# Optimization experiments

Measured on AMD Instinct MI355X. Metric: run time of the kernel, lower is better.

The kernel has to match this reference:

```python
import jax, jax.numpy as jnp
import numpy as np

P = 7    # pool size (hard-coded in module)
DS = 16  # downsample rate


def _hat_int(t):
    # antiderivative of the bilinear hat kernel max(0, 1-|t|)
    t = jnp.clip(t, -1.0, 1.0)
    return jnp.where(t < 0, 0.5 * (t + 1.0) ** 2, 1.0 - 0.5 * (1.0 - t) ** 2)


def _axis_weights(lo, hi, size):
    # Exact per-pixel integration weights for PrRoIPool along one axis.
    # lo, hi: [R] scaled roi coords. Returns W [R,P,size], bin width [R].
    bw = (hi - lo) / P
    starts = lo[:, None] + bw[:, None] * jnp.arange(P, dtype=lo.dtype)  # [R,P]
    ends = starts + bw[:, None]
    idx = jnp.arange(size, dtype=lo.dtype)
    W = _hat_int(ends[:, :, None] - idx) - _hat_int(starts[:, :, None] - idx)
    return W, bw


def prroi_pool(feat, rois):
    # Precise RoI pooling: exact integral of the bilinearly-interpolated feature
    # over each bin (separable -> two small matmuls). feat [C,H,W], rois [R,4].
    C, H, Wd = feat.shape
    s = 1.0 / DS
    Wx, bw = _axis_weights(rois[:, 0] * s, rois[:, 2] * s, Wd)
    Wy, bh = _axis_weights(rois[:, 1] * s, rois[:, 3] * s, H)
    pooled = jnp.einsum('chw,rph,rqw->rcpq', feat, Wy, Wx)  # [R,C,P,P]
    area = jnp.maximum(bw * bh, 1e-8)
    return pooled / area[:, None, None, None]


def intersection_map(box1, box2):
    # Fractional coverage of each PxP bin of box2's grid by box1 -> [N,1,P,P]
    bw = (box2[:, 2] - box2[:, 0]) / P
    bh = (box2[:, 3] - box2[:, 1]) / P
    gx0 = box2[:, 0, None] + bw[:, None] * jnp.arange(P)
    gy0 = box2[:, 1, None] + bh[:, None] * jnp.arange(P)
    ox = jnp.clip(jnp.minimum(gx0 + bw[:, None], box1[:, 2, None]) - jnp.maximum(gx0, box1[:, 0, None]), 0.0)
    oy = jnp.clip(jnp.minimum(gy0 + bh[:, None], box1[:, 3, None]) - jnp.maximum(gy0, box1[:, 1, None]), 0.0)
    frac = oy[:, :, None] * ox[:, None, :] / jnp.maximum(bw * bh, 1e-8)[:, None, None]
    return frac[:, None]


def conv1x1(x, W, b):
    # 1x1 conv as a channel matmul; x [...,C,H,W], W [D,C], b [D]
    return jnp.einsum('...chw,dc->...dhw', x, W) + b[:, None, None]


def setup_inputs() -> dict:
    key = jax.random.key(0)
    ks = jax.random.split(key, 12)
    B, C, Hf, Wf, n = 8, 256, 32, 32, 16
    D1 = D2 = 256
    inp = jax.random.normal(ks[0], (B, C, Hf, Wf), dtype=jnp.float32)
    N = B * n
    xy1 = jax.random.uniform(ks[1], (N, 2), dtype=jnp.float32) * 380.0
    wh = 40.0 + jax.random.uniform(ks[2], (N, 2), dtype=jnp.float32) * 90.0
    objects = jnp.concatenate([xy1, xy1 + wh], axis=-1)  # valid boxes inside 512x512
    objects_length = jnp.full((B,), n, dtype=jnp.int32)

    def kaiming(k, shape, fan_in):
        return jax.random.normal(k, shape, dtype=jnp.float32) * np.float32(np.sqrt(2.0 / fan_in))

    rin = C // 2 * 3 + 2 * D1
    return {
        'input': inp, 'objects': objects, 'objects_length': objects_length,
        'Wc': kaiming(ks[3], (C, C), C), 'bc': jnp.zeros((C,), jnp.float32),
        'Wr': kaiming(ks[4], (C // 2 * 3, C), C), 'br': jnp.zeros((C // 2 * 3,), jnp.float32),
        'Wof': kaiming(ks[5], (D1, 2 * C), 2 * C), 'bof': jnp.zeros((D1,), jnp.float32),
        'Wrf': kaiming(ks[6], (D2, rin), rin), 'brf': jnp.zeros((D2,), jnp.float32),
        'Wofc': kaiming(ks[7], (D1, D1 * P * P), D1 * P * P), 'bofc': jnp.zeros((D1,), jnp.float32),
        'Wrfc': kaiming(ks[8], (D2, D2 * P * P), D2 * P * P), 'brfc': jnp.zeros((D2,), jnp.float32),
    }


def reference(input, objects, objects_length, Wc, bc, Wr, br, Wof, bof, Wrf, brf, Wofc, bofc, Wrfc, brfc):
    B, C, H, Wd = input.shape
    n = objects.shape[0] // B  # uniform object count per image
    boxes = objects.reshape(B, n, 4)
    ctx_all = conv1x1(input, Wc, bc)           # [B,C,H,W]
    rel_all = conv1x1(input, Wr, br)           # [B,3C/2,H,W]
    img_box = jnp.array([0.0, 0.0, Wd * DS, H * DS], dtype=input.dtype)
    sub_id = jnp.repeat(jnp.arange(n), n)
    obj_id = jnp.tile(jnp.arange(n), n)

    def per_image(feat, ctx, rel, box):
        # context pooled over the full-image box is identical for all objects
        ctx_pool = prroi_pool(ctx, img_box[None])[0]                    # [C,P,P]
        x_c, y_c = jnp.split(ctx_pool, 2, axis=0)
        box_imap = jax.lax.stop_gradient(
            intersection_map(box, jnp.broadcast_to(img_box, (n, 4))))  # [n,1,P,P]
        obj_pool = prroi_pool(feat, box)                                # [n,C,P,P]
        obj_in = jnp.concatenate([
            obj_pool,
            jnp.broadcast_to(x_c, (n,) + x_c.shape),
            y_c[None] * box_imap], axis=1)                              # [n,2C,P,P]
        obj_feat = conv1x1(obj_in, Wof, bof)                            # [n,D1,P,P]

        sub_box, ob_box = box[sub_id], box[obj_id]                      # [n*n,4]
        union = jax.lax.stop_gradient(jnp.concatenate(
            [jnp.minimum(sub_box[:, :2], ob_box[:, :2]),
             jnp.maximum(sub_box[:, 2:], ob_box[:, 2:])], axis=-1))
        sub_imap = jax.lax.stop_gradient(intersection_map(sub_box, union))
        obj_imap = jax.lax.stop_gradient(intersection_map(ob_box, union))
        rel_pool = prroi_pool(rel, union)                               # [n*n,3C/2,P,P]
        xr, yr, zr = jnp.split(rel_pool, 3, axis=1)
        rel_in = jnp.concatenate([
            obj_feat[sub_id], obj_feat[obj_id],
            xr, yr * sub_imap, zr * obj_imap], axis=1)                  # [n*n,2D1+3C/2,P,P]
        rel_feat = conv1x1(rel_in, Wrf, brf)                            # [n*n,D2,P,P]

        o = jax.nn.relu(obj_feat).reshape(n, -1) @ Wofc.T + bofc
        o = o / jnp.linalg.norm(o, axis=-1, keepdims=True)
        r = jax.nn.relu(rel_feat).reshape(n * n, -1) @ Wrfc.T + brfc
        r = r / jnp.linalg.norm(r, axis=-1, keepdims=True)
        return o, r.reshape(n, n, -1)

    obj_out, rel_out = jax.vmap(per_image)(input, ctx_all, rel_all, boxes)
    return obj_out, rel_out
```

## Files before the change

### kernel.cpp

```cpp
#include <hip/hip_runtime.h>
#include <hip/hip_bf16.h>


#define Bimg 8
#define Cch 256
#define HW 1024
#define CREL 384
#define CCAT 640
#define KFC 12544
#define STS 236

typedef __hip_bfloat16 bf16;
typedef __attribute__((ext_vector_type(8))) short short8;
typedef __attribute__((ext_vector_type(4))) short short4_t;
typedef __attribute__((ext_vector_type(4))) float f32x4;

__device__ __forceinline__ float hat_int(float t) {
    t = fminf(1.f, fmaxf(-1.f, t));
    return (t < 0.f) ? 0.5f * (t + 1.f) * (t + 1.f) : 1.f - 0.5f * (1.f - t) * (1.f - t);
}
__device__ __forceinline__ float b2f(short s) {
    return __uint_as_float(((unsigned)(unsigned short)s) << 16);
}
__device__ __forceinline__ unsigned pack2bf(float a, float b) {
    bf16 ha = __float2bfloat16(a), hb = __float2bfloat16(b);
    return ((unsigned)(unsigned short)(*(short*)&hb) << 16) | (unsigned short)(*(short*)&ha);
}
__device__ __forceinline__ void u2pair(int u, int& oi, int& oj) {
    int ii = 0, base = 0;
    while (u >= base + 16 - ii) { base += 16 - ii; ii++; }
    oi = ii; oj = ii + (u - base);
}

__global__ void prep_k(const float* __restrict__ Wc, const float* __restrict__ bc,
                       const float* __restrict__ Wr, const float* __restrict__ br,
                       bf16* __restrict__ Wcat, float* __restrict__ bcat,
                       const float* __restrict__ Wof, bf16* __restrict__ wof16,
                       const float* __restrict__ Wrf, bf16* __restrict__ wasao16,
                       bf16* __restrict__ wrfxyz16) {
    int bid = blockIdx.x, tid = threadIdx.x;
    if (bid < 640) {
        int t = bid * 256 + tid;
        int d = t >> 8, c = t & 255;
        Wcat[t] = __float2bfloat16((d < 256) ? Wc[d * 256 + c] : Wr[(d - 256) * 256 + c]);
        if (t < CCAT) bcat[t] = (t < 256) ? bc[t] : br[t - 256];
    } else if (bid < 1152) {
        int t = (bid - 640) * 256 + tid;
        wof16[t] = __float2bfloat16(Wof[t]);
    } else if (bid < 1664) {
        int t = (bid - 1152) * 256 + tid;
        int m = t >> 8, k = t & 255;
        wasao16[t] = __float2bfloat16((m < 256) ? Wrf[m * 896 + k] : Wrf[(m - 256) * 896 + 256 + k]);
    } else {
        int t = (bid - 1664) * 256 + tid;
        int d = t / 384, k = t - d * 384;
        wrfxyz16[t] = __float2bfloat16(Wrf[d * 896 + 512 + k]);
    }
}
__global__ __launch_bounds__(256) void wfc_pack_k(const float* __restrict__ W, bf16* __restrict__ dst) {
    __shared__ float ld[64 * 50];
    int dout = blockIdx.y, d0 = blockIdx.x * 64;
    int tid = threadIdx.x;
    for (int e = tid; e < 64 * 49; e += 256) {
        int di = e / 49, pq = e - di * 49;
        ld[di * 50 + pq] = W[(size_t)dout * KFC + (d0 + di) * 49 + pq];
    }
    __syncthreads();
    for (int e = tid; e < 64 * 49; e += 256) {
        int pq = e >> 6, di = e & 63;
        if (pq < 49)
            dst[(size_t)dout * KFC + pq * 256 + d0 + di] = __float2bfloat16(ld[di * 50 + pq]);
    }
}

__global__ void axisw_k(const float* __restrict__ objects,
                        float* __restrict__ orec, float* __restrict__ urec,
                        float* __restrict__ crec, float* __restrict__ bimap) {
    int bid = blockIdx.x;
    float b0, b1, b2, b3;
    float* rec;
    const float *sbp = nullptr, *obp = nullptr;
    if (bid < 128) {
        b0 = objects[bid * 4]; b1 = objects[bid * 4 + 1];
        b2 = objects[bid * 4 + 2]; b3 = objects[bid * 4 + 3];
        rec = orec + (size_t)bid * 128;
    } else if (bid < 2176) {
        int u = bid - 128;
        int img = u >> 8, pair = u & 255, i = pair >> 4, j = pair & 15;
        sbp = objects + (img * 16 + i) * 4;
        obp = objects + (img * 16 + j) * 4;
        b0 = fminf(sbp[0], obp[0]); b1 = fminf(sbp[1], obp[1]);
        b2 = fmaxf(sbp[2], obp[2]); b3 = fmaxf(sbp[3], obp[3]);
        rec = urec + (size_t)(u) * 224;
    } else {
        b0 = 0.f; b1 = 0.f; b2 = 512.f; b3 = 512.f;
        rec = crec;
    }
    const float sc = 0.0625f;
    float lox = b0 * sc, bwx = (b2 * sc - lox) * (1.f / 7.f);
    float loy = b1 * sc, bwy = (b3 * sc - loy) * (1.f / 7.f);
    float ia = 1.f / fmaxf(bwx * bwy, 1e-8f);
    int tid = threadIdx.x;
    if (tid < 56) {
        int p = tid >> 3, k = tid & 7;
        {
            float st = loy + bwy * p, en = st + bwy;
            int h0 = min(max((int)floorf(st) - 1, 0), 24);
            rec[tid] = hat_int(en - (float)(h0 + k)) - hat_int(st - (float)(h0 + k));
            if (k == 0) ((int*)rec)[119 + p] = h0;
        }
        {
            float st = lox + bwx * p, en = st + bwx;
            int w0 = min(max((int)floorf(st) - 1, 0), 24);
            rec[56 + tid] = ia * (hat_int(en - (float)(w0 + k)) - hat_int(st - (float)(w0 + k)));
            if (k == 0) ((int*)rec)[112 + p] = w0;
        }
    }
    if (tid < 49) {
        int p = tid / 7, q = tid - p * 7;
        if (bid < 128) {
            float bw = 512.f / 7.f, bh = 512.f / 7.f;
            float gx0 = bw * q, gy0 = bh * p;
            float ox = fmaxf(fminf(gx0 + bw, b2) - fmaxf(gx0, b0), 0.f);
            float oy = fmaxf(fminf(gy0 + bh, b3) - fmaxf(gy0, b1), 0.f);
            bimap[bid * 49 + tid] = oy * ox / fmaxf(bw * bh, 1e-8f);
        } else if (bid < 2176) {
            float bw = (b2 - b0) * (1.f / 7.f), bh = (b3 - b1) * (1.f / 7.f);
            float gx0 = b0 + bw * q, gy0 = b1 + bh * p;
            float inv = 1.f / fmaxf(bw * bh, 1e-8f);
            float oxs = fmaxf(fminf(gx0 + bw, sbp[2]) - fmaxf(gx0, sbp[0]), 0.f);
            float oys = fmaxf(fminf(gy0 + bh, sbp[3]) - fmaxf(gy0, sbp[1]), 0.f);
            rec[126 + tid] = oys * oxs * inv;
            float oxo = fmaxf(fminf(gx0 + bw, obp[2]) - fmaxf(gx0, obp[0]), 0.f);
            float oyo = fmaxf(fminf(gy0 + bh, obp[3]) - fmaxf(gy0, obp[1]), 0.f);
            rec[175 + tid] = oyo * oxo * inv;
        }
    }
}

__global__ __launch_bounds__(256) void int_t_k(const float* __restrict__ input, bf16* __restrict__ intp) {
    __shared__ float st[64][65];
    int hw0 = blockIdx.x * 64, c0 = blockIdx.y * 64, b = blockIdx.z;
    int tid = threadIdx.x;
#pragma unroll
    for (int i = 0; i < 16; i++) {
        int e = tid + i * 256;
        int c = e >> 6, hw = e & 63;
        st[c][hw] = input[(size_t)b * 262144 + (size_t)(c0 + c) * 1024 + hw0 + hw];
    }
    __syncthreads();
#pragma unroll
    for (int i = 0; i < 16; i++) {
        int e = tid + i * 256;
        int hw = e >> 6, c = e & 63;
        intp[((size_t)b * 1024 + hw0 + hw) * 256 + c0 + c] = __float2bfloat16(st[c][hw]);
    }
}

__global__ __launch_bounds__(256) void mfma_gemm_k(
    const bf16* __restrict__ A, int lda,
    const bf16* __restrict__ BT, int ldbt,
    int Ktiles, int splitk, int mode,
    float* __restrict__ Cf, int Mtot, int Ntot,
    const float* __restrict__ bias,
    bf16* __restrict__ Ct, int ldct, bf16* __restrict__ Ct2) {
    __shared__ float tr[32 * 132];
    const int tid = threadIdx.x;
    const int m0 = blockIdx.y * 128, n0 = blockIdx.x * 128;
    int kz = blockIdx.z;
    const int tp = (Ktiles + splitk - 1) / splitk;
    const int kt0 = kz * tp;
    const int kt1 = min(Ktiles, kt0 + tp);
    const int lane = tid & 63, wid = tid >> 6;
    const int wm = (wid >> 1) * 64, wn = (wid & 1) * 64;
    const int lrow = lane & 15, lk = (lane >> 4) * 8;
    f32x4 acc[4][4];
#pragma unroll
    for (int i = 0; i < 4; i++)
#pragma unroll
        for (int j = 0; j < 4; j++) acc[i][j] = (f32x4){0.f, 0.f, 0.f, 0.f};
    const bf16* pA = A + (size_t)(m0 + wm + lrow) * lda + lk;
    const bf16* pB = BT + (size_t)(n0 + wn + lrow) * ldbt + lk;
    short8 a_c[4], b_c[4];
    if (kt0 < kt1) {
#pragma unroll
        for (int f = 0; f < 4; f++) {
            a_c[f] = *(const short8*)(pA + (size_t)f * 16 * lda + (size_t)kt0 * 32);
            b_c[f] = *(const short8*)(pB + (size_t)f * 16 * ldbt + (size_t)kt0 * 32);
        }
    }
    for (int kt = kt0; kt < kt1; kt++) {
        short8 a_n[4], b_n[4];
        if (kt + 1 < kt1) {
#pragma unroll
            for (int f = 0; f < 4; f++) {
                a_n[f] = *(const short8*)(pA + (size_t)f * 16 * lda + (size_t)(kt + 1) * 32);
                b_n[f] = *(const short8*)(pB + (size_t)f * 16 * ldbt + (size_t)(kt + 1) * 32);
            }
        }
#pragma unroll
        for (int i = 0; i < 4; i++)
#pragma unroll
            for (int j = 0; j < 4; j++)
                acc[i][j] = __builtin_amdgcn_mfma_f32_16x16x32_bf16(a_c[i], b_c[j], acc[i][j], 0, 0, 0);
#pragma unroll
        for (int f = 0; f < 4; f++) { a_c[f] = a_n[f]; b_c[f] = b_n[f]; }
    }
    const int rbase = (lane >> 4) * 4, cf = lane & 15;
    if (mode == 5) {
#pragma unroll
        for (int i = 0; i < 4; i++)
#pragma unroll
            for (int reg = 0; reg < 4; reg++) {
                int m = m0 + wm + i * 16 + rbase + reg;
                float bv = bias[m];
#pragma unroll
                for (int j = 0; j < 4; j++) {
                    int n = n0 + wn + j * 16 + cf;
                    Ct[(size_t)m * ldct + n] = __float2bfloat16(acc[i][j][reg] + bv);
                }
            }
        return;
    }
#pragma unroll 1
    for (int ci = 0; ci < 4; ci++) {
        __syncthreads();
        if ((wid & 1) == (ci >> 1)) {
            int jj0 = (ci & 1) * 2;
#pragma unroll
            for (int jj = jj0; jj < jj0 + 2; jj++)
#pragma unroll
                for (int i = 0; i < 4; i++)
#pragma unroll
                    for (int reg = 0; reg < 4; reg++) {
                        int nl = (wn + jj * 16 + cf) - 32 * ci;
                        int ml = wm + i * 16 + rbase + reg;
                        tr[nl * 132 + ml] = acc[i][jj][reg];
                    }
        }
        __syncthreads();
        if (mode == 2) {
            float* P = Cf + (size_t)kz * Mtot * Ntot;
            for (int e = tid; e < 1024; e += 256) {
                int nl = e >> 5, mq = (e & 31) * 4;
                int n = n0 + 32 * ci + nl;
                *(f32x4*)&P[(size_t)n * Mtot + m0 + mq] = *(f32x4*)&tr[nl * 132 + mq];
            }
        } else {
            for (int e = tid; e < 2048; e += 256) {
                int nl = e >> 6, mq = (e & 63) * 2;
                int n = n0 + 32 * ci + nl;
                int m = m0 + mq;
                float v0 = tr[nl * 132 + mq] + (bias ? bias[m] : 0.f);
                float v1 = tr[nl * 132 + mq + 1] + (bias ? bias[m + 1] : 0.f);
                *(unsigned*)&Ct[(size_t)n * ldct + m] = pack2bf(v0, v1);
                if (mode == 6) {
                    int r = n / 49, pq = n - r * 49;
                    *(unsigned*)&Ct2[(size_t)r * KFC + pq * 256 + m] =
                        pack2bf(fmaxf(v0, 0.f), fmaxf(v1, 0.f));
                }
            }
        }
    }
}

__global__ __launch_bounds__(256) void mfma_gemm256_k(
    const bf16* __restrict__ A, int lda,
    const bf16* __restrict__ BT, int ldbt, long zB,
    int Ktiles, int splitk, int mode,
    float* __restrict__ Cf, int Ntot,
    const float* __restrict__ bias,
    const bf16* __restrict__ ASAOT, int bimg0,
    bf16* __restrict__ Ct, long zC) {
    __shared__ float tr[16 * 260];
    const int tid = threadIdx.x;
    const int n0 = blockIdx.x * 64;
    int z = blockIdx.z;
    int kz = 0, bimg = bimg0;
    if (mode == 1) { BT += (size_t)z * zB; Ct += (size_t)z * zC; bimg = bimg0 + z; }
    else kz = z;
    const int tp = (Ktiles + splitk - 1) / splitk;
    const int kt0 = kz * tp;
    const int kt1 = min(Ktiles, kt0 + tp);
    const int lane = tid & 63, wid = tid >> 6;
    const int wm = wid * 64;
    const int lrow = lane & 15, lk = (lane >> 4) * 8;
    f32x4 acc[4][4];
#pragma unroll
    for (int i = 0; i < 4; i++)
#pragma unroll
        for (int j = 0; j < 4; j++) acc[i][j] = (f32x4){0.f, 0.f, 0.f, 0.f};
    const bf16* pA = A + (size_t)(wm + lrow) * lda + lk;
    const bf16* pB = (mode == 1)
        ? BT + (size_t)(lk >> 3) * 100352 + (size_t)(n0 + lrow) * 8
        : BT + (size_t)(n0 + lrow) * ldbt + lk;
    short8 a_c[4], b_c[4];
    if (kt0 < kt1) {
#pragma unroll
        for (int f = 0; f < 4; f++) {
            a_c[f] = *(const short8*)(pA + (size_t)f * 16 * lda + (size_t)kt0 * 32);
            b_c[f] = (mode == 1)
                ? *(const short8*)(pB + (size_t)kt0 * 4 * 100352 + f * 128)
                : *(const short8*)(pB + (size_t)f * 16 * ldbt + (size_t)kt0 * 32);
        }
    }
    for (int kt = kt0; kt < kt1; kt++) {
        short8 a_n[4], b_n[4];
        if (kt + 1 < kt1) {
#pragma unroll
            for (int f = 0; f < 4; f++) {
                a_n[f] = *(const short8*)(pA + (size_t)f * 16 * lda + (size_t)(kt + 1) * 32);
                b_n[f] = (mode == 1)
                    ? *(const short8*)(pB + (size_t)(kt + 1) * 4 * 100352 + f * 128)
                    : *(const short8*)(pB + (size_t)f * 16 * ldbt + (size_t)(kt + 1) * 32);
            }
        }
#pragma unroll
        for (int i = 0; i < 4; i++)
#pragma unroll
            for (int j = 0; j < 4; j++)
                acc[i][j] = __builtin_amdgcn_mfma_f32_16x16x32_bf16(a_c[i], b_c[j], acc[i][j], 0, 0, 0);
#pragma unroll
        for (int f = 0; f < 4; f++) { a_c[f] = a_n[f]; b_c[f] = b_n[f]; }
    }
    const int rbase = (lane >> 4) * 4, cf = lane & 15;
#pragma unroll 1
    for (int ci = 0; ci < 4; ci++) {
        __syncthreads();
#pragma unroll
        for (int i = 0; i < 4; i++)
#pragma unroll
            for (int reg = 0; reg < 4; reg++)
                tr[cf * 260 + wm + i * 16 + rbase + reg] = acc[i][ci][reg];
        __syncthreads();
        if (mode == 2) {
            float* P = Cf + (size_t)kz * 256 * Ntot;
            for (int e = tid; e < 1024; e += 256) {
                int nl = e >> 6, mq = (e & 63) * 4;
                int n = n0 + 16 * ci + nl;
                *(f32x4*)&P[(size_t)n * 256 + mq] = *(f32x4*)&tr[nl * 260 + mq];
            }
        } else {
            for (int e = tid; e < 512; e += 256) {
                int nl = e >> 5, mq = (e & 31) * 8;
                int n = n0 + 16 * ci + nl;
                int r = n / 49, pq = n - r * 49;
                int ii = r >> 4, jj2 = r & 15;
                const bf16* as = &ASAOT[((size_t)bimg * 784 + ii * 49 + pq) * 512 + mq];
                const bf16* ao = &ASAOT[((size_t)bimg * 784 + jj2 * 49 + pq) * 512 + 256 + mq];
                short8 pk;
#pragma unroll
                for (int u = 0; u < 8; u++) {
                    float v = tr[nl * 260 + mq + u] + bias[mq + u]
                            + b2f(*(const short*)&as[u]) + b2f(*(const short*)&ao[u]);
                    bf16 h = __float2bfloat16(fmaxf(v, 0.f));
                    pk[u] = *(short*)&h;
                }
                *(short8*)&Ct[(size_t)r * KFC + pq * 256 + mq] = pk;
            }
        }
    }
}

__global__ __launch_bounds__(256) void objpool_k(
    const float* __restrict__ input, const float* __restrict__ orec,
    bf16* __restrict__ objint) {
    int cg = blockIdx.x;
    int b = blockIdx.y;
    __shared__ float sF[8192];
    __shared__ float sT[2][1888];
    __shared__ float wb[2][128];
    int tid = threadIdx.x;
    const float* feat = input + (size_t)b * (Cch * HW) + (size_t)cg * 8 * HW;
    for (int e4 = tid; e4 < 2048; e4 += 256)
        *(f32x4*)&sF[e4 * 4] = *(const f32x4*)&feat[e4 * 4];
    const float* rb = orec + (size_t)b * 16 * 128;
    if (tid < 126) wb[0][tid] = rb[tid];
    int t1v = tid + 256;
    int c0 = tid / 56, r0 = tid - c0 * 56, p0 = r0 >> 3, w40 = r0 & 7;
    int c1 = t1v / 56, r1 = t1v - c1 * 56, p1 = r1 >> 3, w41 = r1 & 7;
    bool has1 = (t1v < 448);
    int sf0 = c0 * 1024 + w40 * 4, st0 = c0 * STS + p0 * 32 + w40 * 4;
    int sf1 = c1 * 1024 + w41 * 4, st1 = c1 * STS + p1 * 32 + w41 * 4;
    int xpq0 = tid >> 3, xc = tid & 7;
    int xp0 = xpq0 / 7, xq0 = xpq0 - xp0 * 7;
    int xpq1 = xpq0 + 32;
    int xp1 = xpq1 / 7, xq1 = xpq1 - xp1 * 7;
    bool xv1 = (xpq1 < 49);
    __syncthreads();
    for (int r2 = 0; r2 < 16; r2++) {
        const float* wc_ = wb[r2 & 1];
        float* stbuf = sT[r2 & 1];
        float pre;
        bool pf = (r2 < 15) && (tid < 126);
        if (pf) pre = rb[(r2 + 1) * 128 + tid];
        {
            int h0 = ((const int*)wc_)[119 + p0];
            const f32x4* f = (const f32x4*)&sF[sf0 + h0 * 32];
            f32x4 wya = *(const f32x4*)&wc_[p0 * 8];
            f32x4 wyb = *(const f32x4*)&wc_[p0 * 8 + 4];
            f32x4 a = f[0] * wya[0] + f[8] * wya[1] + f[16] * wya[2] + f[24] * wya[3]
                    + f[32] * wyb[0] + f[40] * wyb[1] + f[48] * wyb[2] + f[56] * wyb[3];
            *(f32x4*)&stbuf[st0] = a;
        }
        if (has1) {
            int h0 = ((const int*)wc_)[119 + p1];
            const f32x4* f = (const f32x4*)&sF[sf1 + h0 * 32];
            f32x4 wya = *(const f32x4*)&wc_[p1 * 8];
            f32x4 wyb = *(const f32x4*)&wc_[p1 * 8 + 4];
            f32x4 a = f[0] * wya[0] + f[8] * wya[1] + f[16] * wya[2] + f[24] * wya[3]
                    + f[32] * wyb[0] + f[40] * wyb[1] + f[48] * wyb[2] + f[56] * wyb[3];
            *(f32x4*)&stbuf[st1] = a;
        }
        f32x4 xwa0 = *(const f32x4*)&wc_[56 + xq0 * 8];
        f32x4 xwb0 = *(const f32x4*)&wc_[56 + xq0 * 8 + 4];
        int w0i0 = ((const int*)wc_)[112 + xq0];
        f32x4 xwa1 = {0, 0, 0, 0}, xwb1 = {0, 0, 0, 0};
        int w0i1 = 0;
        if (xv1) {
            xwa1 = *(const f32x4*)&wc_[56 + xq1 * 8];
            xwb1 = *(const f32x4*)&wc_[56 + xq1 * 8 + 4];
            w0i1 = ((const int*)wc_)[112 + xq1];
        }
        if (pf) wb[1 - (r2 & 1)][tid] = pre;
        __syncthreads();
        {
            bf16* orow = objint + ((size_t)b * 784 + (size_t)r2 * 49) * 512 + cg * 8 + xc;
            {
                const float* t = &stbuf[xc * STS + xp0 * 32 + w0i0];
                float s = t[0] * xwa0[0] + t[1] * xwa0[1] + t[2] * xwa0[2] + t[3] * xwa0[3]
                        + t[4] * xwb0[0] + t[5] * xwb0[1] + t[6] * xwb0[2] + t[7] * xwb0[3];
                orow[(size_t)xpq0 * 512] = __float2bfloat16(s);
            }
            if (xv1) {
                const float* t = &stbuf[xc * STS + xp1 * 32 + w0i1];
                float s = t[0] * xwa1[0] + t[1] * xwa1[1] + t[2] * xwa1[2] + t[3] * xwa1[3]
                        + t[4] * xwb1[0] + t[5] * xwb1[1] + t[6] * xwb1[2] + t[7] * xwb1[3];
                orow[(size_t)xpq1 * 512] = __float2bfloat16(s);
            }
        }
    }
}

__global__ __launch_bounds__(256) void ctxobjin_k(
    const bf16* __restrict__ ctxrelb, const float* __restrict__ crec,
    const float* __restrict__ bimap, bf16* __restrict__ objint) {
    int cg = blockIdx.x;
    int b = blockIdx.y;
    __shared__ float sF[8192];
    __shared__ float sT[1888];
    __shared__ float wc_[128];
    __shared__ float sBI[784];
    int tid = threadIdx.x;
    for (int e4 = tid; e4 < 2048; e4 += 256) {
        short4_t v = *(const short4_t*)&ctxrelb[(size_t)(cg * 8 + (e4 >> 8)) * 8192 + b * 1024 + (e4 & 255) * 4];
        f32x4 fv = {b2f(v[0]), b2f(v[1]), b2f(v[2]), b2f(v[3])};
        *(f32x4*)&sF[e4 * 4] = fv;
    }
    if (tid < 126) wc_[tid] = crec[tid];
    for (int e = tid; e < 784; e += 256) sBI[e] = bimap[b * 784 + e];
    __syncthreads();
    for (int tt = tid; tt < 448; tt += 256) {
        int c = tt / 56, r = tt - c * 56, p = r >> 3, w4 = r & 7;
        int h0 = ((const int*)wc_)[119 + p];
        const f32x4* f = (const f32x4*)&sF[c * 1024 + w4 * 4 + h0 * 32];
        f32x4 wya = *(const f32x4*)&wc_[p * 8];
        f32x4 wyb = *(const f32x4*)&wc_[p * 8 + 4];
        f32x4 a = f[0] * wya[0] + f[8] * wya[1] + f[16] * wya[2] + f[24] * wya[3]
                + f[32] * wyb[0] + f[40] * wyb[1] + f[48] * wyb[2] + f[56] * wyb[3];
        *(f32x4*)&sT[c * STS + p * 32 + w4 * 4] = a;
    }
    __syncthreads();
    bool scale = (cg >= 16);
    for (int e = tid; e < 392; e += 256) {
        int pq = e >> 3, c = e & 7;
        int p = pq / 7, q = pq - p * 7;
        int w0i = ((const int*)wc_)[112 + q];
        const float* t = &sT[c * STS + p * 32 + w0i];
        const f32x4* wx4 = (const f32x4*)&wc_[56 + q * 8];
        f32x4 a = wx4[0], b2 = wx4[1];
        float s = t[0] * a[0] + t[1] * a[1] + t[2] * a[2] + t[3] * a[3]
                + t[4] * b2[0] + t[5] * b2[1] + t[6] * b2[2] + t[7] * b2[3];
        int j = cg * 8 + c;
        bf16* orow = objint + ((size_t)b * 784 + pq) * 512 + 256 + j;
#pragma unroll
        for (int r = 0; r < 16; r++) {
            float m = scale ? sBI[r * 49 + pq] : 1.f;
            orow[(size_t)r * 49 * 512] = __float2bfloat16(s * m);
        }
    }
}

__global__ __launch_bounds__(256) void relpool_k(
    const bf16* __restrict__ ctxrelb, const float* __restrict__ urec,
    bf16* __restrict__ mbt, int b0) {
    int cg = blockIdx.x;
    int rg = blockIdx.y;
    int zi = blockIdx.z;
    int b = b0 + zi;
    mbt += (size_t)zi * 4816896;
    __shared__ float sF[8192];
    __shared__ float sT[2][1888];
    __shared__ float wb[2][224];
    int tid = threadIdx.x;
    for (int e4 = tid; e4 < 2048; e4 += 256) {
        short4_t v = *(const short4_t*)&ctxrelb[(size_t)(256 + cg * 8 + (e4 >> 8)) * 8192 + b * 1024 + (e4 & 255) * 4];
        f32x4 fv = {b2f(v[0]), b2f(v[1]), b2f(v[2]), b2f(v[3])};
        *(f32x4*)&sF[e4 * 4] = fv;
    }
    const float* rb = urec + (size_t)b * 256 * 224;
    {
        int i0, j0; u2pair(rg * 8, i0, j0);
        if (tid < 224) wb[0][tid] = rb[(size_t)(i0 * 16 + j0) * 224 + tid];
    }
    int t1v = tid + 256;
    int c0 = tid / 56, r0 = tid - c0 * 56, p0 = r0 >> 3, w40 = r0 & 7;
    int c1 = t1v / 56, r1 = t1v - c1 * 56, p1 = r1 >> 3, w41 = r1 & 7;
    bool has1 = (t1v < 448);
    int sf0 = c0 * 1024 + w40 * 4, st0 = c0 * STS + p0 * 32 + w40 * 4;
    int sf1 = c1 * 1024 + w41 * 4, st1 = c1 * STS + p1 * 32 + w41 * 4;
    int xpq0 = tid >> 3, xc = tid & 7;
    int xp0 = xpq0 / 7, xq0 = xpq0 - xp0 * 7;
    int xpq1 = xpq0 + 32;
    int xp1 = xpq1 / 7, xq1 = xpq1 - xp1 * 7;
    bool xv1 = (xpq1 < 49);
    int cglob = cg * 8 + xc;
    int mclass = (cglob >= 256) ? 2 : (cglob >= 128 ? 1 : 0);
    __syncthreads();
    for (int r2 = 0; r2 < 8; r2++) {
        const float* wc_ = wb[r2 & 1];
        float* stbuf = sT[r2 & 1];
        int pi, pj; u2pair(rg * 8 + r2, pi, pj);
        float pre;
        bool pf = (r2 < 7) && (tid < 224);
        if (pf) {
            int ni, nj; u2pair(rg * 8 + r2 + 1, ni, nj);
            pre = rb[(size_t)(ni * 16 + nj) * 224 + tid];
        }
        {
            int h0 = ((const int*)wc_)[119 + p0];
            const f32x4* f = (const f32x4*)&sF[sf0 + h0 * 32];
            f32x4 wya = *(const f32x4*)&wc_[p0 * 8];
            f32x4 wyb = *(const f32x4*)&wc_[p0 * 8 + 4];
            f32x4 a = f[0] * wya[0] + f[8] * wya[1] + f[16] * wya[2] + f[24] * wya[3]
                    + f[32] * wyb[0] + f[40] * wyb[1] + f[48] * wyb[2] + f[56] * wyb[3];
            *(f32x4*)&stbuf[st0] = a;
        }
        if (has1) {
            int h0 = ((const int*)wc_)[119 + p1];
            const f32x4* f = (const f32x4*)&sF[sf1 + h0 * 32];
            f32x4 wya = *(const f32x4*)&wc_[p1 * 8];
            f32x4 wyb = *(const f32x4*)&wc_[p1 * 8 + 4];
            f32x4 a = f[0] * wya[0] + f[8] * wya[1] + f[16] * wya[2] + f[24] * wya[3]
                    + f[32] * wyb[0] + f[40] * wyb[1] + f[48] * wyb[2] + f[56] * wyb[3];
            *(f32x4*)&stbuf[st1] = a;
        }
        f32x4 xwa0 = *(const f32x4*)&wc_[56 + xq0 * 8];
        f32x4 xwb0 = *(const f32x4*)&wc_[56 + xq0 * 8 + 4];
        int w0i0 = ((const int*)wc_)[112 + xq0];
        float si0 = wc_[126 + xpq0], oi0 = wc_[175 + xpq0];
        float mA0 = (mclass == 1) ? si0 : (mclass == 2 ? oi0 : 1.f);
        float mB0 = (mclass == 1) ? oi0 : (mclass == 2 ? si0 : 1.f);
        f32x4 xwa1 = {0, 0, 0, 0}, xwb1 = {0, 0, 0, 0};
        int w0i1 = 0;
        float mA1 = 1.f, mB1 = 1.f;
        if (xv1) {
            xwa1 = *(const f32x4*)&wc_[56 + xq1 * 8];
            xwb1 = *(const f32x4*)&wc_[56 + xq1 * 8 + 4];
            w0i1 = ((const int*)wc_)[112 + xq1];
            float si1 = wc_[126 + xpq1], oi1 = wc_[175 + xpq1];
            mA1 = (mclass == 1) ? si1 : (mclass == 2 ? oi1 : 1.f);
            mB1 = (mclass == 1) ? oi1 : (mclass == 2 ? si1 : 1.f);
        }
        if (pf) wb[1 - (r2 & 1)][tid] = pre;
        __syncthreads();
        {
            int rA = pi * 16 + pj, rB = pj * 16 + pi;
            bf16* baseA = mbt + (size_t)cg * 100352 + (size_t)rA * 392;
            bf16* baseB = mbt + (size_t)cg * 100352 + (size_t)rB * 392;
            bool dual = (pi != pj);
            {
                const float* t = &stbuf[xc * STS + xp0 * 32 + w0i0];
                float s = t[0] * xwa0[0] + t[1] * xwa0[1] + t[2] * xwa0[2] + t[3] * xwa0[3]
                        + t[4] * xwb0[0] + t[5] * xwb0[1] + t[6] * xwb0[2] + t[7] * xwb0[3];
                baseA[xpq0 * 8 + xc] = __float2bfloat16(s * mA0);
                if (dual) baseB[xpq0 * 8 + xc] = __float2bfloat16(s * mB0);
            }
            if (xv1) {
                const float* t = &stbuf[xc * STS + xp1 * 32 + w0i1];
                float s = t[0] * xwa1[0] + t[1] * xwa1[1] + t[2] * xwa1[2] + t[3] * xwa1[3]
                        + t[4] * xwb1[0] + t[5] * xwb1[1] + t[6] * xwb1[2] + t[7] * xwb1[3];
                baseA[xpq1 * 8 + xc] = __float2bfloat16(s * mA1);
                if (dual) baseB[xpq1 * 8 + xc] = __float2bfloat16(s * mB1);
            }
        }
    }
}

__global__ void redns_k(const float* __restrict__ Pd, const float* __restrict__ bias,
                        float* __restrict__ out, int N, int splitk, long outBase) {
    int vec = blockIdx.x, m = threadIdx.x;
    float s = bias[m];
    for (int z = 0; z < splitk; z++) s += Pd[(size_t)z * 256 * N + (size_t)vec * 256 + m];
    float ss = s * s;
    for (int o = 32; o > 0; o >>= 1) ss += __shfl_down(ss, o, 64);
    __shared__ float red[4];
    if ((m & 63) == 0) red[m >> 6] = ss;
    __syncthreads();
    float tot = red[0] + red[1] + red[2] + red[3];
    out[outBase + (size_t)vec * 256 + m] = s / sqrtf(tot);
}

extern "C" void kernel_launch(void* const* d_in, const int* in_sizes, int n_in,
                              void* d_out, int out_size, void* d_ws, size_t ws_size,
                              hipStream_t stream) {
    const float* input = (const float*)d_in[0];
    const float* objects = (const float*)d_in[1];
    const float* Wc = (const float*)d_in[3];
    const float* bc = (const float*)d_in[4];
    const float* Wr = (const float*)d_in[5];
    const float* br = (const float*)d_in[6];
    const float* Wof = (const float*)d_in[7];
    const float* bof = (const float*)d_in[8];
    const float* Wrf = (const float*)d_in[9];
    const float* brf = (const float*)d_in[10];
    const float* Wofc = (const float*)d_in[11];
    const float* bofc = (const float*)d_in[12];
    const float* Wrfc = (const float*)d_in[13];
    const float* brfc = (const float*)d_in[14];
    float* out = (float*)d_out;

    float* w = (float*)d_ws;
    bf16* WCAT16   = (bf16*)(w + 0);
    float* BCAT    = w + 81920;
    bf16* CTXRELB  = (bf16*)(w + 82560);
    float* OREC    = w + 2704000;
    float* UREC    = w + 2720384;
    float* CREC    = w + 3179136;
    float* BIMAP   = w + 3179264;
    bf16* ASAOT16  = (bf16*)(w + 3185536);
    bf16* WRFXYZ16 = (bf16*)(w + 4791168);
    bf16* WRFC16   = (bf16*)(w + 4840320);
    float* OVL     = w + 6445952;
    bf16* INT16    = (bf16*)(OVL + 0);
    bf16* WOF16    = (bf16*)(OVL + 1048576);
    bf16* WASAO16  = (bf16*)(OVL + 1114112);
    bf16* WOFC16   = (bf16*)(OVL + 1179648);
    bf16* OBJINT   = (bf16*)(OVL + 2785280);
    bf16* OBJFT    = (bf16*)(OVL + 4390912);
    bf16* XOT      = (bf16*)(OVL + 5193728);
    float* OPART   = OVL + 5996544;
    bf16* MBT4     = (bf16*)(OVL + 0);
    float* RPART   = OVL + 0;
    bf16* XBT4     = (bf16*)(OVL + 9633792);

    prep_k<<<dim3(2048), 256, 0, stream>>>(Wc, bc, Wr, br, WCAT16, BCAT,
                                           Wof, WOF16, Wrf, WASAO16, WRFXYZ16);
    wfc_pack_k<<<dim3(4, 256), 256, 0, stream>>>(Wrfc, WRFC16);
    wfc_pack_k<<<dim3(4, 256), 256, 0, stream>>>(Wofc, WOFC16);
    axisw_k<<<dim3(2177), 64, 0, stream>>>(objects, OREC, UREC, CREC, BIMAP);
    int_t_k<<<dim3(16, 4, 8), 256, 0, stream>>>(input, INT16);
    mfma_gemm_k<<<dim3(64, 5, 1), 256, 0, stream>>>(WCAT16, 256, INT16, 256, 8, 1, 5,
                                                    nullptr, 640, 8192, BCAT,
                                                    CTXRELB, 8192, nullptr);
    objpool_k<<<dim3(32, 8), 256, 0, stream>>>(input, OREC, OBJINT);
    ctxobjin_k<<<dim3(32, 8), 256, 0, stream>>>(CTXRELB, CREC, BIMAP, OBJINT);
    mfma_gemm_k<<<dim3(49, 2, 1), 256, 0, stream>>>(WOF16, 512, OBJINT, 512, 16, 1, 6,
                                                    nullptr, 256, 6272, bof,
                                                    OBJFT, 256, XOT);
    mfma_gemm_k<<<dim3(49, 4, 1), 256, 0, stream>>>(WASAO16, 256, OBJFT, 256, 8, 1, 3,
                                                    nullptr, 512, 6272, nullptr,
                                                    ASAOT16, 512, nullptr);
    mfma_gemm_k<<<dim3(1, 2, 56), 256, 0, stream>>>(WOFC16, KFC, XOT, KFC, 392, 56, 2,
                                                    OPART, 256, 128, nullptr,
                                                    nullptr, 0, nullptr);
    redns_k<<<dim3(128), 256, 0, stream>>>(OPART, bofc, out, 128, 56, 0L);

    for (int g = 0; g < 2; g++) {
        int b0 = g * 4;
        relpool_k<<<dim3(48, 17, 4), 256, 0, stream>>>(CTXRELB, UREC, MBT4, b0);
        mfma_gemm256_k<<<dim3(196, 1, 4), 256, 0, stream>>>(WRFXYZ16, 384, MBT4, 384, 4816896L,
                                                            12, 1, 1,
                                                            nullptr, KFC, brf,
                                                            ASAOT16, b0, XBT4, 3211264L);
        mfma_gemm256_k<<<dim3(16, 1, 24), 256, 0, stream>>>(WRFC16, KFC, XBT4, KFC, 0L,
                                                            392, 24, 2,
                                                            RPART, 1024, nullptr,
                                                            nullptr, 0, nullptr, 0L);
        redns_k<<<dim3(1024), 256, 0, stream>>>(RPART, brfc, out, 1024, 24,
                                                32768L + (long)g * 262144L);
    }
}
```

Measured before the change: 618.4 us.

## Make relpool per-wave independent and preload all pair weights to drop block barriers

Each wave now handles two channels end to end with its own staging buffer, and all eight pairs' weight rows are loaded into shared memory once up front. This removes the per-pair block-wide barrier and the double-buffered prefetch. In exchange, lanes are partially idle and the output stores become more strided, since each wave covers only two channels of the eight-wide output group.

Result: slower. 648.3 us (+4.8%).

```diff
diff --git a/kernel.cpp b/kernel.cpp
--- a/kernel.cpp
+++ b/kernel.cpp
@@ -500,98 +500,68 @@
     int b = b0 + zi;
     mbt += (size_t)zi * 4816896;
     __shared__ float sF[8192];
-    __shared__ float sT[2][1888];
-    __shared__ float wb[2][224];
+    __shared__ float sT[4][472];
+    __shared__ float sR[8][224];
     int tid = threadIdx.x;
-    for (int e4 = tid; e4 < 2048; e4 += 256) {
-        short4_t v = *(const short4_t*)&ctxrelb[(size_t)(256 + cg * 8 + (e4 >> 8)) * 8192 + b * 1024 + (e4 & 255) * 4];
+    int lane = tid & 63, wave = tid >> 6;
+    int c0w = wave * 2;
+    for (int e4 = lane; e4 < 512; e4 += 64) {
+        int ch = e4 >> 8, pos = (e4 & 255) * 4;
+        short4_t v = *(const short4_t*)&ctxrelb[(size_t)(256 + cg * 8 + c0w + ch) * 8192 + b * 1024 + pos];
         f32x4 fv = {b2f(v[0]), b2f(v[1]), b2f(v[2]), b2f(v[3])};
-        *(f32x4*)&sF[e4 * 4] = fv;
+        *(f32x4*)&sF[(c0w + ch) * 1024 + pos] = fv;
     }
     const float* rb = urec + (size_t)b * 256 * 224;
-    {
-        int i0, j0; u2pair(rg * 8, i0, j0);
-        if (tid < 224) wb[0][tid] = rb[(size_t)(i0 * 16 + j0) * 224 + tid];
-    }
-    int t1v = tid + 256;
-    int c0 = tid / 56, r0 = tid - c0 * 56, p0 = r0 >> 3, w40 = r0 & 7;
-    int c1 = t1v / 56, r1 = t1v - c1 * 56, p1 = r1 >> 3, w41 = r1 & 7;
-    bool has1 = (t1v < 448);
-    int sf0 = c0 * 1024 + w40 * 4, st0 = c0 * STS + p0 * 32 + w40 * 4;
-    int sf1 = c1 * 1024 + w41 * 4, st1 = c1 * STS + p1 * 32 + w41 * 4;
-    int xpq0 = tid >> 3, xc = tid & 7;
-    int xp0 = xpq0 / 7, xq0 = xpq0 - xp0 * 7;
-    int xpq1 = xpq0 + 32;
-    int xp1 = xpq1 / 7, xq1 = xpq1 - xp1 * 7;
-    bool xv1 = (xpq1 < 49);
-    int cglob = cg * 8 + xc;
-    int mclass = (cglob >= 256) ? 2 : (cglob >= 128 ? 1 : 0);
+    for (int e = tid; e < 1792; e += 256) {
+        int pp = e / 224, t = e - pp * 224;
+        int i, j; u2pair(rg * 8 + pp, i, j);
+        sR[pp][t] = rb[(size_t)(i * 16 + j) * 224 + t];
+    }
     __syncthreads();
-    for (int r2 = 0; r2 < 8; r2++) {
-        const float* wc_ = wb[r2 & 1];
-        float* stbuf = sT[r2 & 1];
-        int pi, pj; u2pair(rg * 8 + r2, pi, pj);
-        float pre;
-        bool pf = (r2 < 7) && (tid < 224);
-        if (pf) {
-            int ni, nj; u2pair(rg * 8 + r2 + 1, ni, nj);
-            pre = rb[(size_t)(ni * 16 + nj) * 224 + tid];
-        }
-        {
-            int h0 = ((const int*)wc_)[119 + p0];
-            const f32x4* f = (const f32x4*)&sF[sf0 + h0 * 32];
-            f32x4 wya = *(const f32x4*)&wc_[p0 * 8];
-            f32x4 wyb = *(const f32x4*)&wc_[p0 * 8 + 4];
-            f32x4 a = f[0] * wya[0] + f[8] * wya[1] + f[16] * wya[2] + f[24] * wya[3]
-                    + f[32] * wyb[0] + f[40] * wyb[1] + f[48] * wyb[2] + f[56] * wyb[3];
-            *(f32x4*)&stbuf[st0] = a;
-        }
-        if (has1) {
-            int h0 = ((const int*)wc_)[119 + p1];
-            const f32x4* f = (const f32x4*)&sF[sf1 + h0 * 32];
-            f32x4 wya = *(const f32x4*)&wc_[p1 * 8];
-            f32x4 wyb = *(const f32x4*)&wc_[p1 * 8 + 4];
-            f32x4 a = f[0] * wya[0] + f[8] * wya[1] + f[16] * wya[2] + f[24] * wya[3]
-                    + f[32] * wyb[0] + f[40] * wyb[1] + f[48] * wyb[2] + f[56] * wyb[3];
-            *(f32x4*)&stbuf[st1] = a;
-        }
-        f32x4 xwa0 = *(const f32x4*)&wc_[56 + xq0 * 8];
-        f32x4 xwb0 = *(const f32x4*)&wc_[56 + xq0 * 8 + 4];
-        int w0i0 = ((const int*)wc_)[112 + xq0];
-        float si0 = wc_[126 + xpq0], oi0 = wc_[175 + xpq0];
-        float mA0 = (mclass == 1) ? si0 : (mclass == 2 ? oi0 : 1.f);
-        float mB0 = (mclass == 1) ? oi0 : (mclass == 2 ? si0 : 1.f);
-        f32x4 xwa1 = {0, 0, 0, 0}, xwb1 = {0, 0, 0, 0};
-        int w0i1 = 0;
-        float mA1 = 1.f, mB1 = 1.f;
-        if (xv1) {
-            xwa1 = *(const f32x4*)&wc_[56 + xq1 * 8];
-            xwb1 = *(const f32x4*)&wc_[56 + xq1 * 8 + 4];
-            w0i1 = ((const int*)wc_)[112 + xq1];
-            float si1 = wc_[126 + xpq1], oi1 = wc_[175 + xpq1];
-            mA1 = (mclass == 1) ? si1 : (mclass == 2 ? oi1 : 1.f);
-            mB1 = (mclass == 1) ? oi1 : (mclass == 2 ? si1 : 1.f);
-        }
-        if (pf) wb[1 - (r2 & 1)][tid] = pre;
-        __syncthreads();
-        {
-            int rA = pi * 16 + pj, rB = pj * 16 + pi;
-            bf16* baseA = mbt + (size_t)cg * 100352 + (size_t)rA * 392;
-            bf16* baseB = mbt + (size_t)cg * 100352 + (size_t)rB * 392;
-            bool dual = (pi != pj);
-            {
-                const float* t = &stbuf[xc * STS + xp0 * 32 + w0i0];
-                float s = t[0] * xwa0[0] + t[1] * xwa0[1] + t[2] * xwa0[2] + t[3] * xwa0[3]
-                        + t[4] * xwb0[0] + t[5] * xwb0[1] + t[6] * xwb0[2] + t[7] * xwb0[3];
-                baseA[xpq0 * 8 + xc] = __float2bfloat16(s * mA0);
-                if (dual) baseB[xpq0 * 8 + xc] = __float2bfloat16(s * mB0);
-            }
-            if (xv1) {
-                const float* t = &stbuf[xc * STS + xp1 * 32 + w0i1];
-                float s = t[0] * xwa1[0] + t[1] * xwa1[1] + t[2] * xwa1[2] + t[3] * xwa1[3]
-                        + t[4] * xwb1[0] + t[5] * xwb1[1] + t[6] * xwb1[2] + t[7] * xwb1[3];
-                baseA[xpq1 * 8 + xc] = __float2bfloat16(s * mA1);
-                if (dual) baseB[xpq1 * 8 + xc] = __float2bfloat16(s * mB1);
+    float* sTw = sT[wave];
+#pragma unroll 1
+    for (int pp = 0; pp < 8; pp++) {
+        const float* wcr = sR[pp];
+        int pi, pj; u2pair(rg * 8 + pp, pi, pj);
+#pragma unroll
+        for (int it = 0; it < 2; it++) {
+            int t = lane + it * 64;
+            if (t < 112) {
+                int chl = t / 56, r = t - chl * 56;
+                int p = r >> 3, w4 = r & 7;
+                int h0 = ((const int*)wcr)[119 + p];
+                const f32x4* f = (const f32x4*)&sF[(c0w + chl) * 1024 + w4 * 4 + h0 * 32];
+                f32x4 wya = *(const f32x4*)&wcr[p * 8];
+                f32x4 wyb = *(const f32x4*)&wcr[p * 8 + 4];
+                f32x4 a = f[0] * wya[0] + f[8] * wya[1] + f[16] * wya[2] + f[24] * wya[3]
+                        + f[32] * wyb[0] + f[40] * wyb[1] + f[48] * wyb[2] + f[56] * wyb[3];
+                *(f32x4*)&sTw[chl * STS + p * 32 + w4 * 4] = a;
+            }
+        }
+        int rA = pi * 16 + pj, rB = pj * 16 + pi;
+        bf16* baseA = mbt + (size_t)cg * 100352 + (size_t)rA * 392;
+        bf16* baseB = mbt + (size_t)cg * 100352 + (size_t)rB * 392;
+        bool dual = (pi != pj);
+#pragma unroll
+        for (int it = 0; it < 2; it++) {
+            int o = lane + it * 64;
+            if (o < 98) {
+                int chl = o / 49, pq = o - chl * 49;
+                int c = c0w + chl;
+                int p = pq / 7, q = pq - p * 7;
+                int w0i = ((const int*)wcr)[112 + q];
+                const float* t = &sTw[chl * STS + p * 32 + w0i];
+                const f32x4* wx4 = (const f32x4*)&wcr[56 + q * 8];
+                f32x4 a = wx4[0], b2 = wx4[1];
+                float s = t[0] * a[0] + t[1] * a[1] + t[2] * a[2] + t[3] * a[3]
+                        + t[4] * b2[0] + t[5] * b2[1] + t[6] * b2[2] + t[7] * b2[3];
+                int cglob = cg * 8 + c;
+                int mclass = (cglob >= 256) ? 2 : (cglob >= 128 ? 1 : 0);
+                float si = wcr[126 + pq], oi = wcr[175 + pq];
+                float mA = (mclass == 1) ? si : (mclass == 2 ? oi : 1.f);
+                float mB = (mclass == 1) ? oi : (mclass == 2 ? si : 1.f);
+                baseA[pq * 8 + c] = __float2bfloat16(s * mA);
+                if (dual) baseB[pq * 8 + c] = __float2bfloat16(s * mB);
             }
         }
     }
```
